# Performance work log

Hardware: AMD Instinct MI355X
Metric: run time of the kernel (lower is better)

The kernel has to match this reference:

```python
import jax, jax.numpy as jnp
import numpy as np

N = 100000
E = 1000000
C = 64      # hidden_channels
H = 4       # heads
O = C // H  # out channels per head
NEG_SLOPE = 0.2


def setup_inputs() -> dict:
    key = jax.random.key(0)
    ks = jax.random.split(key, 14)
    x = jax.random.normal(ks[0], (N, C), dtype=jnp.float32)
    edge_index = jax.random.randint(ks[1], (2, E), 0, N, dtype=jnp.int64)
    s = 1.0 / np.sqrt(C)
    params = {}
    for l in range(3):
        params[f"Wl{l+1}"] = jax.random.normal(ks[2 + 4 * l], (C, H * O), dtype=jnp.float32) * s
        params[f"Wr{l+1}"] = jax.random.normal(ks[3 + 4 * l], (C, H * O), dtype=jnp.float32) * s
        params[f"a{l+1}"] = jax.random.normal(ks[4 + 4 * l], (H, O), dtype=jnp.float32) * s
        params[f"b{l+1}"] = jnp.zeros((H * O,), dtype=jnp.float32)
    return {"x": x, "edge_index": edge_index, **params}


def _gatv2_layer(x, src, dst, Wl, Wr, a, b):
    # x: [N, C]; src/dst: [E]
    xl = (x @ Wl).reshape(N, H, O)  # source-side transform
    xr = (x @ Wr).reshape(N, H, O)  # target-side transform
    s = jax.nn.leaky_relu(xl[src] + xr[dst], NEG_SLOPE)     # [E, H, O]
    e = jnp.einsum("eho,ho->eh", s, a)                       # [E, H] logits
    # segment softmax over incoming edges of each target node
    m = jax.ops.segment_max(e, dst, num_segments=N)          # [N, H]
    ex = jnp.exp(e - m[dst])
    denom = jax.ops.segment_sum(ex, dst, num_segments=N)     # [N, H]
    alpha = ex / (denom[dst] + 1e-16)                        # [E, H]
    out = jax.ops.segment_sum(xl[src] * alpha[:, :, None], dst, num_segments=N)
    return out.reshape(N, H * O) + b


def reference(x, edge_index, Wl1, Wr1, a1, b1, Wl2, Wr2, a2, b2, Wl3, Wr3, a3, b3):
    src, dst = edge_index[0], edge_index[1]
    h = jax.nn.relu(_gatv2_layer(x, src, dst, Wl1, Wr1, a1, b1))
    h = jax.nn.relu(_gatv2_layer(h, src, dst, Wl2, Wr2, a2, b2))
    h = _gatv2_layer(h, src, dst, Wl3, Wr3, a3, b3)
    return h
```

## Files before the change

### kernel.cpp

```cpp
#include <hip/hip_runtime.h>
#include <math.h>

#define SLOPE 0.2f
#define LOG2E 1.4426950408889634f

#define DPP_ADD(x, ctrl) \
    ((x) + __int_as_float(__builtin_amdgcn_update_dpp( \
        0, __float_as_int(x), (ctrl), 0xF, 0xF, true)))


#define NPB 256
#define EPB 8192
#define MAXBK 2048

__global__ __launch_bounds__(256) void kH1(const int* __restrict__ ei,
                                           int* __restrict__ hist,
                                           int E, int nbk, int nblkE) {
    __shared__ int h[MAXBK];
    int t = threadIdx.x, b = blockIdx.x;
    for (int i = t; i < nbk; i += 256) h[i] = 0;
    __syncthreads();
    int e0 = b * EPB, e1 = min(e0 + EPB, E);
    for (int e = e0 + t; e < e1; e += 256)
        atomicAdd(&h[ei[E + e] >> 8], 1);
    __syncthreads();
    for (int i = t; i < nbk; i += 256)
        hist[i * nblkE + b] = h[i];
}

__global__ __launch_bounds__(256) void kH2(const int* __restrict__ ei,
                                           const int* __restrict__ hs,
                                           int* __restrict__ pairs,
                                           int E, int nbk, int nblkE) {
    __shared__ int soff[MAXBK];
    int t = threadIdx.x, b = blockIdx.x;
    for (int i = t; i < nbk; i += 256) soff[i] = hs[i * nblkE + b];
    __syncthreads();
    int e0 = b * EPB, e1 = min(e0 + EPB, E);
    for (int e = e0 + t; e < e1; e += 256) {
        int s = ei[e], d = ei[E + e];
        int slot = atomicAdd(&soff[d >> 8], 1);
        pairs[slot] = (s << 8) | (d & (NPB - 1));
    }
}

__global__ __launch_bounds__(256) void kB3(const int* __restrict__ hs,
                                           const int* __restrict__ pairs,
                                           int* __restrict__ btot,
                                           int E, int nbk, int nblkE) {
    __shared__ int sdeg[NPB];
    __shared__ int red[256];
    int t = threadIdx.x, b = blockIdx.x;
    sdeg[t] = 0;
    __syncthreads();
    int s0 = hs[b * nblkE];
    int s1 = (b + 1 < nbk) ? hs[(b + 1) * nblkE] : E;
    for (int i = s0 + t; i < s1; i += 256)
        atomicAdd(&sdeg[pairs[i] & (NPB - 1)], 1);
    __syncthreads();
    red[t] = (sdeg[t] + 3) & ~3;
    __syncthreads();
    for (int off = 128; off; off >>= 1) {
        if (t < off) red[t] += red[t + off];
        __syncthreads();
    }
    if (t == 0) btot[b] = red[0];
}

__global__ __launch_bounds__(256) void kscanB(const int* __restrict__ btot,
                                              int* __restrict__ bbase, int nbk) {
    __shared__ int sd[256];
    __shared__ int carry;
    int t = threadIdx.x;
    if (t == 0) carry = 0;
    __syncthreads();
    for (int base = 0; base < nbk; base += 256) {
        int v = (base + t < nbk) ? btot[base + t] : 0;
        sd[t] = v;
        __syncthreads();
        for (int off = 1; off < 256; off <<= 1) {
            int x = (t >= off) ? sd[t - off] : 0;
            __syncthreads();
            sd[t] += x;
            __syncthreads();
        }
        if (base + t < nbk) bbase[base + t] = sd[t] - v + carry;
        __syncthreads();
        if (t == 255) carry += sd[255];
        __syncthreads();
    }
}

__global__ __launch_bounds__(256) void kB4(const int* __restrict__ hs,
                                           const int* __restrict__ pairs,
                                           const int* __restrict__ bbase,
                                           int* __restrict__ rp,
                                           int* __restrict__ deg,
                                           int* __restrict__ col,
                                           int E, int nbk, int nblkE, int n) {
    __shared__ int sdeg[NPB];
    __shared__ int spfx[NPB];
    int t = threadIdx.x, b = blockIdx.x;
    sdeg[t] = 0;
    __syncthreads();
    int s0 = hs[b * nblkE];
    int s1 = (b + 1 < nbk) ? hs[(b + 1) * nblkE] : E;
    for (int i = s0 + t; i < s1; i += 256)
        atomicAdd(&sdeg[pairs[i] & (NPB - 1)], 1);
    __syncthreads();
    int cnt = sdeg[t];
    int pv = (cnt + 3) & ~3;
    spfx[t] = pv;
    __syncthreads();
    for (int off = 1; off < 256; off <<= 1) {
        int x = (t >= off) ? spfx[t - off] : 0;
        __syncthreads();
        spfx[t] += x;
        __syncthreads();
    }
    int rpt = bbase[b] + spfx[t] - pv;
    int node = b * NPB + t;
    if (node < n) { rp[node] = rpt; deg[node] = cnt; }
    __syncthreads();
    sdeg[t] = rpt;
    __syncthreads();
    for (int i = s0 + t; i < s1; i += 256) {
        int p = pairs[i];
        int slot = atomicAdd(&sdeg[p & (NPB - 1)], 1);
        col[slot] = p & ~(NPB - 1);
    }
}


__global__ __launch_bounds__(256) void k_scan1(const int* __restrict__ deg,
                                               int* __restrict__ rp,
                                               int* __restrict__ blk, int n) {
    __shared__ int sd[256];
    int t = threadIdx.x;
    int base = blockIdx.x * 1024 + t * 4;
    int v0 = 0, v1 = 0, v2 = 0, v3 = 0;
    if (base + 0 < n) v0 = deg[base + 0];
    if (base + 1 < n) v1 = deg[base + 1];
    if (base + 2 < n) v2 = deg[base + 2];
    if (base + 3 < n) v3 = deg[base + 3];
    int s = v0 + v1 + v2 + v3;
    sd[t] = s;
    __syncthreads();
    for (int off = 1; off < 256; off <<= 1) {
        int x = (t >= off) ? sd[t - off] : 0;
        __syncthreads();
        sd[t] += x;
        __syncthreads();
    }
    int ex = sd[t] - s;
    if (t == 255) blk[blockIdx.x] = sd[255];
    if (base + 0 < n) rp[base + 0] = ex; ex += v0;
    if (base + 1 < n) rp[base + 1] = ex; ex += v1;
    if (base + 2 < n) rp[base + 2] = ex; ex += v2;
    if (base + 3 < n) rp[base + 3] = ex;
}

__global__ __launch_bounds__(256) void k_scan2(int* __restrict__ blk, int nblk) {
    __shared__ int sd[256];
    int t = threadIdx.x;
    int v = (t < nblk) ? blk[t] : 0;
    sd[t] = v;
    __syncthreads();
    for (int off = 1; off < 256; off <<= 1) {
        int x = (t >= off) ? sd[t - off] : 0;
        __syncthreads();
        sd[t] += x;
        __syncthreads();
    }
    if (t < nblk) blk[t] = sd[t] - v;
}

__global__ __launch_bounds__(256) void k_scan3(int* __restrict__ rp,
                                               const int* __restrict__ blk,
                                               int n) {
    int t = threadIdx.x;
    int base = blockIdx.x * 1024 + t * 4;
    int off = blk[blockIdx.x];
    #pragma unroll
    for (int i = 0; i < 4; i++) {
        int idx = base + i;
        if (idx < n) rp[idx] += off;
    }
}


__global__ __launch_bounds__(256) void k_gemm(const float* __restrict__ in,
                                              const float* __restrict__ Wl,
                                              const float* __restrict__ Wr,
                                              float* __restrict__ xl,
                                              float* __restrict__ xr, int n) {
    __shared__ float4 sW[64 * 32];
    __shared__ float  sx[64 * 68];

    int t = threadIdx.x;
    int base = blockIdx.x * 64;

    float4 xs[4];
    int xrow[4], xkq[4];
    #pragma unroll
    for (int s = 0; s < 4; s++) {
        int i = t + 256 * s;
        int row = i >> 4, kq = i & 15;
        int g = base + row;
        if (g > n - 1) g = n - 1;
        xs[s] = *(const float4*)(in + (size_t)g * 64 + kq * 4);
        xrow[s] = row; xkq[s] = kq;
    }
    for (int i = t; i < 2048; i += 256) {
        int k = i >> 5, jg = i & 31;
        const float* src = (jg < 16) ? (Wl + k * 64 + jg * 4)
                                     : (Wr + k * 64 + (jg - 16) * 4);
        sW[i] = *(const float4*)src;
    }
    #pragma unroll
    for (int s = 0; s < 4; s++)
        *(float4*)(sx + xrow[s] * 68 + xkq[s] * 4) = xs[s];
    __syncthreads();

    int rt = t & 15;
    int ct = t >> 4;
    const float* sxp = sx + rt * 68;

    float4 acc[4][2];
    #pragma unroll
    for (int r = 0; r < 4; r++)
        #pragma unroll
        for (int j = 0; j < 2; j++) acc[r][j] = make_float4(0.f, 0.f, 0.f, 0.f);

    #pragma unroll 1
    for (int k0 = 0; k0 < 64; k0 += 4) {
        float4 xv[4];
        #pragma unroll
        for (int r = 0; r < 4; r++)
            xv[r] = *(const float4*)(sxp + r * (16 * 68) + k0);
        #pragma unroll
        for (int kk = 0; kk < 4; kk++) {
            float4 w0 = sW[(k0 + kk) * 32 + ct * 2 + 0];
            float4 w1 = sW[(k0 + kk) * 32 + ct * 2 + 1];
            #pragma unroll
            for (int r = 0; r < 4; r++) {
                float xk = (kk == 0) ? xv[r].x : (kk == 1) ? xv[r].y
                         : (kk == 2) ? xv[r].z : xv[r].w;
                acc[r][0].x += xk * w0.x;
                acc[r][0].y += xk * w0.y;
                acc[r][0].z += xk * w0.z;
                acc[r][0].w += xk * w0.w;
                acc[r][1].x += xk * w1.x;
                acc[r][1].y += xk * w1.y;
                acc[r][1].z += xk * w1.z;
                acc[r][1].w += xk * w1.w;
            }
        }
    }

    float* outh = (ct < 8) ? xl : xr;
    int cq = (ct & 7) * 8;
    #pragma unroll
    for (int r = 0; r < 4; r++) {
        int g = base + rt + 16 * r;
        if (g < n) {
            float* dst = outh + (size_t)g * 64 + cq;
            *(float4*)(dst + 0) = acc[r][0];
            *(float4*)(dst + 4) = acc[r][1];
        }
    }
}


__global__ __launch_bounds__(256) void k_node(const float* __restrict__ xl,
                                              const float* __restrict__ xr,
                                              const int* __restrict__ rp,
                                              const int* __restrict__ deg,
                                              const int* __restrict__ col,
                                              const float* __restrict__ A,
                                              const float* __restrict__ Bv,
                                              float* __restrict__ outp,
                                              int n, int relu) {
    int lane = threadIdx.x & 63;
    int node = __builtin_amdgcn_readfirstlane(blockIdx.x * 4 + (threadIdx.x >> 6));
    if (node >= n) return;
    int grp = lane >> 5;
    int s   = lane & 31;
    int chn = ((s >> 3) << 4) + ((s & 7) << 1);
    unsigned cofs = (unsigned)chn * 4u;

    float2 xr2 = *(const float2*)(xr + (size_t)node * 64 + chn);
    float2 a2  = *(const float2*)(A + chn);
    a2.x *= LOG2E; a2.y *= LOG2E;
    float2 b2  = *(const float2*)(Bv + chn);

    int start = rp[node];
    int d = deg[node];
    int nb = (d + 7) >> 3;
    const int* cp = col + start;
    const char* xlb = (const char*)xl;

    float den = 0.f;
    float ax = 0.f, ay = 0.f;

    auto batch = [&](const float2 (&v)[4], int ebase, bool full) {
        #pragma unroll
        for (int j = 0; j < 4; j++) {
            float sx_ = v[j].x + xr2.x;
            float sy_ = v[j].y + xr2.y;
            sx_ = fmaxf(sx_, SLOPE * sx_);
            sy_ = fmaxf(sy_, SLOPE * sy_);
            float q = sx_ * a2.x + sy_ * a2.y;
            q = DPP_ADD(q, 0xB1);
            q = DPP_ADD(q, 0x4E);
            q = DPP_ADD(q, 0x141);
            if (!full) {
                int eidx = ebase + 2 * j + grp;
                if (eidx >= d) q = -INFINITY;
            }
            float w = __builtin_amdgcn_exp2f(q);
            den += w;
            ax += w * v[j].x;
            ay += w * v[j].y;
        }
    };

    auto gather = [&](float2 (&v)[4], const int* q) {
        int c[8];
        *(int4*)(c + 0) = *(const int4*)(q + 0);
        *(int4*)(c + 4) = *(const int4*)(q + 4);
        #pragma unroll
        for (int j = 0; j < 4; j++) {
            unsigned cc = (unsigned)(grp ? c[2 * j + 1] : c[2 * j]);
            v[j] = *(const float2*)(xlb + (cc + cofs));
        }
    };

    float2 v[4];
    if (nb > 0) gather(v, cp);

    #pragma unroll 1
    for (int b = 0; b < nb - 1; b++) {
        float2 vN[4];
        gather(vN, cp + (b + 1) * 8);
        batch(v, b * 8, true);
        #pragma unroll
        for (int j = 0; j < 4; j++) v[j] = vN[j];
    }
    if (nb > 0) batch(v, (nb - 1) * 8, false);

    den += __shfl_xor(den, 32, 64);
    ax  += __shfl_xor(ax, 32, 64);
    ay  += __shfl_xor(ay, 32, 64);

    float inv = 1.f / (den + 1e-16f);
    float ox = ax * inv + b2.x;
    float oy = ay * inv + b2.y;
    if (relu) { ox = fmaxf(ox, 0.f); oy = fmaxf(oy, 0.f); }
    if (grp == 0)
        *(float2*)(outp + (size_t)node * 64 + chn) = make_float2(ox, oy);
}


extern "C" void kernel_launch(void* const* d_in, const int* in_sizes, int n_in,
                              void* d_out, int out_size, void* d_ws, size_t ws_size,
                              hipStream_t stream) {
    const float* x = (const float*)d_in[0];
    const int* ei = (const int*)d_in[1];
    int N = in_sizes[0] / 64;
    int E = in_sizes[1] / 2;

    const float* Wl[3] = {(const float*)d_in[2], (const float*)d_in[6], (const float*)d_in[10]};
    const float* Wr[3] = {(const float*)d_in[3], (const float*)d_in[7], (const float*)d_in[11]};
    const float* Av[3] = {(const float*)d_in[4], (const float*)d_in[8], (const float*)d_in[12]};
    const float* Bv[3] = {(const float*)d_in[5], (const float*)d_in[9], (const float*)d_in[13]};

    char* w = (char*)d_ws;
    auto carve = [&](size_t bytes) {
        void* p = (void*)w;
        w += (bytes + 255) & ~(size_t)255;
        return p;
    };
    int NBK    = (N + NPB - 1) / NPB;
    int NBLK_E = (E + EPB - 1) / EPB;
    size_t histN = (size_t)NBK * NBLK_E;
    size_t colN = (size_t)E + 3 * (size_t)N + 64;
    float* xl    = (float*)carve((size_t)N * 64 * 4);
    float* xr    = (float*)carve((size_t)N * 64 * 4);
    float* h     = (float*)carve((size_t)N * 64 * 4);
    int*   rp    = (int*)carve((size_t)N * 4);
    int*   deg   = (int*)carve((size_t)N * 4);
    int*   col   = (int*)carve(colN * 4);
    int*   pairs = (int*)carve((size_t)E * 4);
    int*   hist  = (int*)carve(histN * 4);
    int*   hs    = (int*)carve(histN * 4);
    int*   btot  = (int*)carve((size_t)NBK * 4);
    int*   bbase = (int*)carve((size_t)NBK * 4);
    int*   blkB  = (int*)carve(256 * 4);

    int nblkH1024 = (int)((histN + 1023) / 1024);
    int gemm_grid = (N + 63) / 64;
    int node_grid = (N + 3) / 4;

    hipMemsetAsync(col, 0, colN * 4, stream);

    kH1<<<NBLK_E, 256, 0, stream>>>(ei, hist, E, NBK, NBLK_E);
    k_scan1<<<nblkH1024, 256, 0, stream>>>(hist, hs, blkB, (int)histN);
    k_scan2<<<1, 256, 0, stream>>>(blkB, nblkH1024);
    k_scan3<<<nblkH1024, 256, 0, stream>>>(hs, blkB, (int)histN);
    kH2<<<NBLK_E, 256, 0, stream>>>(ei, hs, pairs, E, NBK, NBLK_E);

    kB3<<<NBK, 256, 0, stream>>>(hs, pairs, btot, E, NBK, NBLK_E);
    kscanB<<<1, 256, 0, stream>>>(btot, bbase, NBK);
    kB4<<<NBK, 256, 0, stream>>>(hs, pairs, bbase, rp, deg, col, E, NBK, NBLK_E, N);

    const float* in_l = x;
    for (int l = 0; l < 3; l++) {
        float* out_l = (l == 2) ? (float*)d_out : h;
        int relu = (l < 2) ? 1 : 0;
        k_gemm<<<gemm_grid, 256, 0, stream>>>(in_l, Wl[l], Wr[l], xl, xr, N);
        k_node<<<node_grid, 256, 0, stream>>>(xl, xr, rp, deg, col, Av[l], Bv[l],
                                              out_l, N, relu);
        in_l = h;
    }
}
```

Measured before the change: 359.6 us.

## Fuse CSR construction into one cooperative kernel with grid syncs

Replaces the eight-kernel CSR build (histogram, three-pass scan, scatter, per-bucket degree, bucket scan, final placement) and the col memset with a single cooperative kernel of 1024 blocks that uses grid.sync between phases. Padding of the per-node column lists changes from multiples of 4 to 16, and the padding slots are zeroed in-kernel instead of by a full memset. This is meant to remove launch gaps and the memset traffic, at the cost of grid-wide barriers, a fixed grid size, and more padding in col. The histogram scan now assumes nbk blocks each covering 1024 entries, which matches nbk*1024 hist entries.

```diff
diff --git a/kernel.cpp b/kernel.cpp
--- a/kernel.cpp
+++ b/kernel.cpp
@@ -1,5 +1,8 @@
 #include <hip/hip_runtime.h>
+#include <hip/hip_cooperative_groups.h>
 #include <math.h>
+
+namespace cg = cooperative_groups;
 
 #define SLOPE 0.2f
 #define LOG2E 1.4426950408889634f
@@ -10,181 +13,165 @@
 
 
 #define NPB 256
-#define EPB 8192
 #define MAXBK 2048
-
-__global__ __launch_bounds__(256) void kH1(const int* __restrict__ ei,
-                                           int* __restrict__ hist,
-                                           int E, int nbk, int nblkE) {
+#define CSRG 1024
+
+__global__ __launch_bounds__(256) void k_csr(const int* __restrict__ ei,
+                                             int* __restrict__ pairs,
+                                             int* __restrict__ hist,
+                                             int* __restrict__ blk,
+                                             int* __restrict__ btot,
+                                             int* __restrict__ bbase,
+                                             int* __restrict__ rp,
+                                             int* __restrict__ deg,
+                                             int* __restrict__ col,
+                                             int E, int nbk, int n) {
+    cg::grid_group grid = cg::this_grid();
     __shared__ int h[MAXBK];
+    __shared__ int sd[256];
+    __shared__ int carry;
+    __shared__ int sdeg[NPB];
+    __shared__ int spfx[NPB];
+
     int t = threadIdx.x, b = blockIdx.x;
+    int G = CSRG;
+    int chunk = (E + G - 1) / G;
+    int e0 = b * chunk, e1 = min(e0 + chunk, E);
+
     for (int i = t; i < nbk; i += 256) h[i] = 0;
     __syncthreads();
-    int e0 = b * EPB, e1 = min(e0 + EPB, E);
     for (int e = e0 + t; e < e1; e += 256)
         atomicAdd(&h[ei[E + e] >> 8], 1);
     __syncthreads();
     for (int i = t; i < nbk; i += 256)
-        hist[i * nblkE + b] = h[i];
-}
-
-__global__ __launch_bounds__(256) void kH2(const int* __restrict__ ei,
-                                           const int* __restrict__ hs,
-                                           int* __restrict__ pairs,
-                                           int E, int nbk, int nblkE) {
-    __shared__ int soff[MAXBK];
-    int t = threadIdx.x, b = blockIdx.x;
-    for (int i = t; i < nbk; i += 256) soff[i] = hs[i * nblkE + b];
+        hist[i * G + b] = h[i];
+    grid.sync();
+
+    if (b < nbk) {
+        int base = b * 1024 + t * 4;
+        int v0 = hist[base], v1 = hist[base + 1];
+        int v2 = hist[base + 2], v3 = hist[base + 3];
+        int s = v0 + v1 + v2 + v3;
+        sd[t] = s;
+        __syncthreads();
+        for (int off = 1; off < 256; off <<= 1) {
+            int x = (t >= off) ? sd[t - off] : 0;
+            __syncthreads();
+            sd[t] += x;
+            __syncthreads();
+        }
+        int ex = sd[t] - s;
+        if (t == 255) blk[b] = sd[255];
+        hist[base] = ex; ex += v0;
+        hist[base + 1] = ex; ex += v1;
+        hist[base + 2] = ex; ex += v2;
+        hist[base + 3] = ex;
+    }
+    grid.sync();
+
+    if (b == 0) {
+        if (t == 0) carry = 0;
+        __syncthreads();
+        for (int base = 0; base < nbk; base += 256) {
+            int v = (base + t < nbk) ? blk[base + t] : 0;
+            sd[t] = v;
+            __syncthreads();
+            for (int off = 1; off < 256; off <<= 1) {
+                int x = (t >= off) ? sd[t - off] : 0;
+                __syncthreads();
+                sd[t] += x;
+                __syncthreads();
+            }
+            if (base + t < nbk) blk[base + t] = sd[t] - v + carry;
+            __syncthreads();
+            if (t == 255) carry += sd[255];
+            __syncthreads();
+        }
+    }
+    grid.sync();
+
+    if (b < nbk) {
+        int base = b * 1024 + t * 4;
+        int o = blk[b];
+        hist[base] += o; hist[base + 1] += o;
+        hist[base + 2] += o; hist[base + 3] += o;
+    }
+    grid.sync();
+
+    for (int i = t; i < nbk; i += 256) h[i] = hist[i * G + b];
     __syncthreads();
-    int e0 = b * EPB, e1 = min(e0 + EPB, E);
     for (int e = e0 + t; e < e1; e += 256) {
         int s = ei[e], d = ei[E + e];
-        int slot = atomicAdd(&soff[d >> 8], 1);
+        int slot = atomicAdd(&h[d >> 8], 1);
         pairs[slot] = (s << 8) | (d & (NPB - 1));
     }
-}
-
-__global__ __launch_bounds__(256) void kB3(const int* __restrict__ hs,
-                                           const int* __restrict__ pairs,
-                                           int* __restrict__ btot,
-                                           int E, int nbk, int nblkE) {
-    __shared__ int sdeg[NPB];
-    __shared__ int red[256];
-    int t = threadIdx.x, b = blockIdx.x;
-    sdeg[t] = 0;
-    __syncthreads();
-    int s0 = hs[b * nblkE];
-    int s1 = (b + 1 < nbk) ? hs[(b + 1) * nblkE] : E;
-    for (int i = s0 + t; i < s1; i += 256)
-        atomicAdd(&sdeg[pairs[i] & (NPB - 1)], 1);
-    __syncthreads();
-    red[t] = (sdeg[t] + 3) & ~3;
-    __syncthreads();
-    for (int off = 128; off; off >>= 1) {
-        if (t < off) red[t] += red[t + off];
-        __syncthreads();
-    }
-    if (t == 0) btot[b] = red[0];
-}
-
-__global__ __launch_bounds__(256) void kscanB(const int* __restrict__ btot,
-                                              int* __restrict__ bbase, int nbk) {
-    __shared__ int sd[256];
-    __shared__ int carry;
-    int t = threadIdx.x;
-    if (t == 0) carry = 0;
-    __syncthreads();
-    for (int base = 0; base < nbk; base += 256) {
-        int v = (base + t < nbk) ? btot[base + t] : 0;
-        sd[t] = v;
+    grid.sync();
+
+    if (b < nbk) {
+        sdeg[t] = 0;
+        __syncthreads();
+        int s0 = hist[b * G];
+        int s1 = (b + 1 < nbk) ? hist[(b + 1) * G] : E;
+        for (int i = s0 + t; i < s1; i += 256)
+            atomicAdd(&sdeg[pairs[i] & (NPB - 1)], 1);
+        __syncthreads();
+        spfx[t] = (sdeg[t] + 15) & ~15;
+        __syncthreads();
+        for (int off = 128; off; off >>= 1) {
+            if (t < off) spfx[t] += spfx[t + off];
+            __syncthreads();
+        }
+        if (t == 0) btot[b] = spfx[0];
+    }
+    grid.sync();
+
+    if (b == 0) {
+        if (t == 0) carry = 0;
+        __syncthreads();
+        for (int base = 0; base < nbk; base += 256) {
+            int v = (base + t < nbk) ? btot[base + t] : 0;
+            sd[t] = v;
+            __syncthreads();
+            for (int off = 1; off < 256; off <<= 1) {
+                int x = (t >= off) ? sd[t - off] : 0;
+                __syncthreads();
+                sd[t] += x;
+                __syncthreads();
+            }
+            if (base + t < nbk) bbase[base + t] = sd[t] - v + carry;
+            __syncthreads();
+            if (t == 255) carry += sd[255];
+            __syncthreads();
+        }
+    }
+    grid.sync();
+
+    if (b < nbk) {
+        int cnt = sdeg[t];
+        int pv = (cnt + 15) & ~15;
+        spfx[t] = pv;
         __syncthreads();
         for (int off = 1; off < 256; off <<= 1) {
-            int x = (t >= off) ? sd[t - off] : 0;
-            __syncthreads();
-            sd[t] += x;
-            __syncthreads();
-        }
-        if (base + t < nbk) bbase[base + t] = sd[t] - v + carry;
-        __syncthreads();
-        if (t == 255) carry += sd[255];
-        __syncthreads();
-    }
-}
-
-__global__ __launch_bounds__(256) void kB4(const int* __restrict__ hs,
-                                           const int* __restrict__ pairs,
-                                           const int* __restrict__ bbase,
-                                           int* __restrict__ rp,
-                                           int* __restrict__ deg,
-                                           int* __restrict__ col,
-                                           int E, int nbk, int nblkE, int n) {
-    __shared__ int sdeg[NPB];
-    __shared__ int spfx[NPB];
-    int t = threadIdx.x, b = blockIdx.x;
-    sdeg[t] = 0;
-    __syncthreads();
-    int s0 = hs[b * nblkE];
-    int s1 = (b + 1 < nbk) ? hs[(b + 1) * nblkE] : E;
-    for (int i = s0 + t; i < s1; i += 256)
-        atomicAdd(&sdeg[pairs[i] & (NPB - 1)], 1);
-    __syncthreads();
-    int cnt = sdeg[t];
-    int pv = (cnt + 3) & ~3;
-    spfx[t] = pv;
-    __syncthreads();
-    for (int off = 1; off < 256; off <<= 1) {
-        int x = (t >= off) ? spfx[t - off] : 0;
-        __syncthreads();
-        spfx[t] += x;
-        __syncthreads();
-    }
-    int rpt = bbase[b] + spfx[t] - pv;
-    int node = b * NPB + t;
-    if (node < n) { rp[node] = rpt; deg[node] = cnt; }
-    __syncthreads();
-    sdeg[t] = rpt;
-    __syncthreads();
-    for (int i = s0 + t; i < s1; i += 256) {
-        int p = pairs[i];
-        int slot = atomicAdd(&sdeg[p & (NPB - 1)], 1);
-        col[slot] = p & ~(NPB - 1);
-    }
-}
-
-
-__global__ __launch_bounds__(256) void k_scan1(const int* __restrict__ deg,
-                                               int* __restrict__ rp,
-                                               int* __restrict__ blk, int n) {
-    __shared__ int sd[256];
-    int t = threadIdx.x;
-    int base = blockIdx.x * 1024 + t * 4;
-    int v0 = 0, v1 = 0, v2 = 0, v3 = 0;
-    if (base + 0 < n) v0 = deg[base + 0];
-    if (base + 1 < n) v1 = deg[base + 1];
-    if (base + 2 < n) v2 = deg[base + 2];
-    if (base + 3 < n) v3 = deg[base + 3];
-    int s = v0 + v1 + v2 + v3;
-    sd[t] = s;
-    __syncthreads();
-    for (int off = 1; off < 256; off <<= 1) {
-        int x = (t >= off) ? sd[t - off] : 0;
-        __syncthreads();
-        sd[t] += x;
-        __syncthreads();
-    }
-    int ex = sd[t] - s;
-    if (t == 255) blk[blockIdx.x] = sd[255];
-    if (base + 0 < n) rp[base + 0] = ex; ex += v0;
-    if (base + 1 < n) rp[base + 1] = ex; ex += v1;
-    if (base + 2 < n) rp[base + 2] = ex; ex += v2;
-    if (base + 3 < n) rp[base + 3] = ex;
-}
-
-__global__ __launch_bounds__(256) void k_scan2(int* __restrict__ blk, int nblk) {
-    __shared__ int sd[256];
-    int t = threadIdx.x;
-    int v = (t < nblk) ? blk[t] : 0;
-    sd[t] = v;
-    __syncthreads();
-    for (int off = 1; off < 256; off <<= 1) {
-        int x = (t >= off) ? sd[t - off] : 0;
-        __syncthreads();
-        sd[t] += x;
-        __syncthreads();
-    }
-    if (t < nblk) blk[t] = sd[t] - v;
-}
-
-__global__ __launch_bounds__(256) void k_scan3(int* __restrict__ rp,
-                                               const int* __restrict__ blk,
-                                               int n) {
-    int t = threadIdx.x;
-    int base = blockIdx.x * 1024 + t * 4;
-    int off = blk[blockIdx.x];
-    #pragma unroll
-    for (int i = 0; i < 4; i++) {
-        int idx = base + i;
-        if (idx < n) rp[idx] += off;
+            int x = (t >= off) ? spfx[t - off] : 0;
+            __syncthreads();
+            spfx[t] += x;
+            __syncthreads();
+        }
+        int rpt = bbase[b] + spfx[t] - pv;
+        int node = b * NPB + t;
+        if (node < n) { rp[node] = rpt; deg[node] = cnt; }
+        __syncthreads();
+        sdeg[t] = rpt;
+        __syncthreads();
+        int s0 = hist[b * G];
+        int s1 = (b + 1 < nbk) ? hist[(b + 1) * G] : E;
+        for (int i = s0 + t; i < s1; i += 256) {
+            int p = pairs[i];
+            int slot = atomicAdd(&sdeg[p & (NPB - 1)], 1);
+            col[slot] = p & ~(NPB - 1);
+        }
+        if (node < n)
+            for (int i = rpt + cnt; i < rpt + pv; i++) col[i] = 0;
     }
 }
 
@@ -381,10 +368,9 @@
         w += (bytes + 255) & ~(size_t)255;
         return p;
     };
-    int NBK    = (N + NPB - 1) / NPB;
-    int NBLK_E = (E + EPB - 1) / EPB;
-    size_t histN = (size_t)NBK * NBLK_E;
-    size_t colN = (size_t)E + 3 * (size_t)N + 64;
+    int NBK = (N + NPB - 1) / NPB;
+    size_t histN = (size_t)NBK * CSRG;
+    size_t colN = (size_t)E + 15 * (size_t)N + 64;
     float* xl    = (float*)carve((size_t)N * 64 * 4);
     float* xr    = (float*)carve((size_t)N * 64 * 4);
     float* h     = (float*)carve((size_t)N * 64 * 4);
@@ -393,26 +379,18 @@
     int*   col   = (int*)carve(colN * 4);
     int*   pairs = (int*)carve((size_t)E * 4);
     int*   hist  = (int*)carve(histN * 4);
-    int*   hs    = (int*)carve(histN * 4);
+    int*   blk   = (int*)carve((size_t)MAXBK * 4);
     int*   btot  = (int*)carve((size_t)NBK * 4);
     int*   bbase = (int*)carve((size_t)NBK * 4);
-    int*   blkB  = (int*)carve(256 * 4);
-
-    int nblkH1024 = (int)((histN + 1023) / 1024);
+
     int gemm_grid = (N + 63) / 64;
     int node_grid = (N + 3) / 4;
 
-    hipMemsetAsync(col, 0, colN * 4, stream);
-
-    kH1<<<NBLK_E, 256, 0, stream>>>(ei, hist, E, NBK, NBLK_E);
-    k_scan1<<<nblkH1024, 256, 0, stream>>>(hist, hs, blkB, (int)histN);
-    k_scan2<<<1, 256, 0, stream>>>(blkB, nblkH1024);
-    k_scan3<<<nblkH1024, 256, 0, stream>>>(hs, blkB, (int)histN);
-    kH2<<<NBLK_E, 256, 0, stream>>>(ei, hs, pairs, E, NBK, NBLK_E);
-
-    kB3<<<NBK, 256, 0, stream>>>(hs, pairs, btot, E, NBK, NBLK_E);
-    kscanB<<<1, 256, 0, stream>>>(btot, bbase, NBK);
-    kB4<<<NBK, 256, 0, stream>>>(hs, pairs, bbase, rp, deg, col, E, NBK, NBLK_E, N);
+    void* csr_args[] = {(void*)&ei, (void*)&pairs, (void*)&hist, (void*)&blk,
+                        (void*)&btot, (void*)&bbase, (void*)&rp, (void*)&deg,
+                        (void*)&col, (void*)&E, (void*)&NBK, (void*)&N};
+    hipLaunchCooperativeKernel((void*)k_csr, dim3(CSRG), dim3(256),
+                               csr_args, 0, stream);
 
     const float* in_l = x;
     for (int l = 0; l < 3; l++) {
```

Measured after the change: 1.094 ms. 204% more time.

## Fold single-block scans into consumers, drop col memset, pad rows to 16

Applied to the files above, without the earlier changes.

Removes the two single-block scan kernels (k_scan2, kscanB) by having each block of k_scan3 and kB4 reduce the preceding block totals itself, cutting kernel launches and serial tiny-kernel stages. Replaces the full hipMemsetAsync of col by having kB4 zero only its own padding slots. Row padding grows from multiples of 4 to multiples of 16, which enlarges col and adds padded work in the node kernel, possibly to suit a wider per-node edge loop.

```diff
diff --git a/kernel.cpp b/kernel.cpp
--- a/kernel.cpp
+++ b/kernel.cpp
@@ -27,110 +27,6 @@
     for (int i = t; i < nbk; i += 256)
         hist[i * nblkE + b] = h[i];
 }
-
-__global__ __launch_bounds__(256) void kH2(const int* __restrict__ ei,
-                                           const int* __restrict__ hs,
-                                           int* __restrict__ pairs,
-                                           int E, int nbk, int nblkE) {
-    __shared__ int soff[MAXBK];
-    int t = threadIdx.x, b = blockIdx.x;
-    for (int i = t; i < nbk; i += 256) soff[i] = hs[i * nblkE + b];
-    __syncthreads();
-    int e0 = b * EPB, e1 = min(e0 + EPB, E);
-    for (int e = e0 + t; e < e1; e += 256) {
-        int s = ei[e], d = ei[E + e];
-        int slot = atomicAdd(&soff[d >> 8], 1);
-        pairs[slot] = (s << 8) | (d & (NPB - 1));
-    }
-}
-
-__global__ __launch_bounds__(256) void kB3(const int* __restrict__ hs,
-                                           const int* __restrict__ pairs,
-                                           int* __restrict__ btot,
-                                           int E, int nbk, int nblkE) {
-    __shared__ int sdeg[NPB];
-    __shared__ int red[256];
-    int t = threadIdx.x, b = blockIdx.x;
-    sdeg[t] = 0;
-    __syncthreads();
-    int s0 = hs[b * nblkE];
-    int s1 = (b + 1 < nbk) ? hs[(b + 1) * nblkE] : E;
-    for (int i = s0 + t; i < s1; i += 256)
-        atomicAdd(&sdeg[pairs[i] & (NPB - 1)], 1);
-    __syncthreads();
-    red[t] = (sdeg[t] + 3) & ~3;
-    __syncthreads();
-    for (int off = 128; off; off >>= 1) {
-        if (t < off) red[t] += red[t + off];
-        __syncthreads();
-    }
-    if (t == 0) btot[b] = red[0];
-}
-
-__global__ __launch_bounds__(256) void kscanB(const int* __restrict__ btot,
-                                              int* __restrict__ bbase, int nbk) {
-    __shared__ int sd[256];
-    __shared__ int carry;
-    int t = threadIdx.x;
-    if (t == 0) carry = 0;
-    __syncthreads();
-    for (int base = 0; base < nbk; base += 256) {
-        int v = (base + t < nbk) ? btot[base + t] : 0;
-        sd[t] = v;
-        __syncthreads();
-        for (int off = 1; off < 256; off <<= 1) {
-            int x = (t >= off) ? sd[t - off] : 0;
-            __syncthreads();
-            sd[t] += x;
-            __syncthreads();
-        }
-        if (base + t < nbk) bbase[base + t] = sd[t] - v + carry;
-        __syncthreads();
-        if (t == 255) carry += sd[255];
-        __syncthreads();
-    }
-}
-
-__global__ __launch_bounds__(256) void kB4(const int* __restrict__ hs,
-                                           const int* __restrict__ pairs,
-                                           const int* __restrict__ bbase,
-                                           int* __restrict__ rp,
-                                           int* __restrict__ deg,
-                                           int* __restrict__ col,
-                                           int E, int nbk, int nblkE, int n) {
-    __shared__ int sdeg[NPB];
-    __shared__ int spfx[NPB];
-    int t = threadIdx.x, b = blockIdx.x;
-    sdeg[t] = 0;
-    __syncthreads();
-    int s0 = hs[b * nblkE];
-    int s1 = (b + 1 < nbk) ? hs[(b + 1) * nblkE] : E;
-    for (int i = s0 + t; i < s1; i += 256)
-        atomicAdd(&sdeg[pairs[i] & (NPB - 1)], 1);
-    __syncthreads();
-    int cnt = sdeg[t];
-    int pv = (cnt + 3) & ~3;
-    spfx[t] = pv;
-    __syncthreads();
-    for (int off = 1; off < 256; off <<= 1) {
-        int x = (t >= off) ? spfx[t - off] : 0;
-        __syncthreads();
-        spfx[t] += x;
-        __syncthreads();
-    }
-    int rpt = bbase[b] + spfx[t] - pv;
-    int node = b * NPB + t;
-    if (node < n) { rp[node] = rpt; deg[node] = cnt; }
-    __syncthreads();
-    sdeg[t] = rpt;
-    __syncthreads();
-    for (int i = s0 + t; i < s1; i += 256) {
-        int p = pairs[i];
-        int slot = atomicAdd(&sdeg[p & (NPB - 1)], 1);
-        col[slot] = p & ~(NPB - 1);
-    }
-}
-
 
 __global__ __launch_bounds__(256) void k_scan1(const int* __restrict__ deg,
                                                int* __restrict__ rp,
@@ -160,32 +56,119 @@
     if (base + 3 < n) rp[base + 3] = ex;
 }
 
-__global__ __launch_bounds__(256) void k_scan2(int* __restrict__ blk, int nblk) {
-    __shared__ int sd[256];
-    int t = threadIdx.x;
-    int v = (t < nblk) ? blk[t] : 0;
-    sd[t] = v;
-    __syncthreads();
-    for (int off = 1; off < 256; off <<= 1) {
-        int x = (t >= off) ? sd[t - off] : 0;
-        __syncthreads();
-        sd[t] += x;
-        __syncthreads();
-    }
-    if (t < nblk) blk[t] = sd[t] - v;
-}
-
 __global__ __launch_bounds__(256) void k_scan3(int* __restrict__ rp,
                                                const int* __restrict__ blk,
                                                int n) {
-    int t = threadIdx.x;
-    int base = blockIdx.x * 1024 + t * 4;
-    int off = blk[blockIdx.x];
+    __shared__ int red[256];
+    int t = threadIdx.x, b = blockIdx.x;
+    int v = 0;
+    for (int i = t; i < b; i += 256) v += blk[i];
+    red[t] = v;
+    __syncthreads();
+    for (int off = 128; off; off >>= 1) {
+        if (t < off) red[t] += red[t + off];
+        __syncthreads();
+    }
+    int off0 = red[0];
+    int base = b * 1024 + t * 4;
     #pragma unroll
     for (int i = 0; i < 4; i++) {
         int idx = base + i;
-        if (idx < n) rp[idx] += off;
-    }
+        if (idx < n) rp[idx] += off0;
+    }
+}
+
+__global__ __launch_bounds__(256) void kH2(const int* __restrict__ ei,
+                                           const int* __restrict__ hs,
+                                           int* __restrict__ pairs,
+                                           int E, int nbk, int nblkE) {
+    __shared__ int soff[MAXBK];
+    int t = threadIdx.x, b = blockIdx.x;
+    for (int i = t; i < nbk; i += 256) soff[i] = hs[i * nblkE + b];
+    __syncthreads();
+    int e0 = b * EPB, e1 = min(e0 + EPB, E);
+    for (int e = e0 + t; e < e1; e += 256) {
+        int s = ei[e], d = ei[E + e];
+        int slot = atomicAdd(&soff[d >> 8], 1);
+        pairs[slot] = (s << 8) | (d & (NPB - 1));
+    }
+}
+
+__global__ __launch_bounds__(256) void kB3(const int* __restrict__ hs,
+                                           const int* __restrict__ pairs,
+                                           int* __restrict__ btot,
+                                           int E, int nbk, int nblkE) {
+    __shared__ int sdeg[NPB];
+    __shared__ int red[256];
+    int t = threadIdx.x, b = blockIdx.x;
+    sdeg[t] = 0;
+    __syncthreads();
+    int s0 = hs[b * nblkE];
+    int s1 = (b + 1 < nbk) ? hs[(b + 1) * nblkE] : E;
+    for (int i = s0 + t; i < s1; i += 256)
+        atomicAdd(&sdeg[pairs[i] & (NPB - 1)], 1);
+    __syncthreads();
+    red[t] = (sdeg[t] + 15) & ~15;
+    __syncthreads();
+    for (int off = 128; off; off >>= 1) {
+        if (t < off) red[t] += red[t + off];
+        __syncthreads();
+    }
+    if (t == 0) btot[b] = red[0];
+}
+
+__global__ __launch_bounds__(256) void kB4(const int* __restrict__ hs,
+                                           const int* __restrict__ pairs,
+                                           const int* __restrict__ btot,
+                                           int* __restrict__ rp,
+                                           int* __restrict__ deg,
+                                           int* __restrict__ col,
+                                           int E, int nbk, int nblkE, int n) {
+    __shared__ int sdeg[NPB];
+    __shared__ int spfx[NPB];
+    int t = threadIdx.x, b = blockIdx.x;
+
+    int v = 0;
+    for (int i = t; i < b; i += 256) v += btot[i];
+    spfx[t] = v;
+    __syncthreads();
+    for (int off = 128; off; off >>= 1) {
+        if (t < off) spfx[t] += spfx[t + off];
+        __syncthreads();
+    }
+    int bb = spfx[0];
+    __syncthreads();
+
+    sdeg[t] = 0;
+    __syncthreads();
+    int s0 = hs[b * nblkE];
+    int s1 = (b + 1 < nbk) ? hs[(b + 1) * nblkE] : E;
+    for (int i = s0 + t; i < s1; i += 256)
+        atomicAdd(&sdeg[pairs[i] & (NPB - 1)], 1);
+    __syncthreads();
+    int cnt = sdeg[t];
+    int pv = (cnt + 15) & ~15;
+    spfx[t] = pv;
+    __syncthreads();
+    for (int off = 1; off < 256; off <<= 1) {
+        int x = (t >= off) ? spfx[t - off] : 0;
+        __syncthreads();
+        spfx[t] += x;
+        __syncthreads();
+    }
+    int rpt = bb + spfx[t] - pv;
+    int node = b * NPB + t;
+    if (node < n) { rp[node] = rpt; deg[node] = cnt; }
+    __syncthreads();
+    sdeg[t] = rpt;
+    __syncthreads();
+    for (int i = s0 + t; i < s1; i += 256) {
+        int p = pairs[i];
+        int slot = atomicAdd(&sdeg[p & (NPB - 1)], 1);
+        col[slot] = p & ~(NPB - 1);
+    }
+    if (node < n)
+        for (int i = rpt + cnt; i < rpt + pv; i++) col[i] = 0;
 }
 
 
@@ -384,7 +367,7 @@
     int NBK    = (N + NPB - 1) / NPB;
     int NBLK_E = (E + EPB - 1) / EPB;
     size_t histN = (size_t)NBK * NBLK_E;
-    size_t colN = (size_t)E + 3 * (size_t)N + 64;
+    size_t colN = (size_t)E + 15 * (size_t)N + 64;
     float* xl    = (float*)carve((size_t)N * 64 * 4);
     float* xr    = (float*)carve((size_t)N * 64 * 4);
     float* h     = (float*)carve((size_t)N * 64 * 4);
@@ -395,24 +378,19 @@
     int*   hist  = (int*)carve(histN * 4);
     int*   hs    = (int*)carve(histN * 4);
     int*   btot  = (int*)carve((size_t)NBK * 4);
-    int*   bbase = (int*)carve((size_t)NBK * 4);
     int*   blkB  = (int*)carve(256 * 4);
 
     int nblkH1024 = (int)((histN + 1023) / 1024);
     int gemm_grid = (N + 63) / 64;
     int node_grid = (N + 3) / 4;
 
-    hipMemsetAsync(col, 0, colN * 4, stream);
-
     kH1<<<NBLK_E, 256, 0, stream>>>(ei, hist, E, NBK, NBLK_E);
     k_scan1<<<nblkH1024, 256, 0, stream>>>(hist, hs, blkB, (int)histN);
-    k_scan2<<<1, 256, 0, stream>>>(blkB, nblkH1024);
     k_scan3<<<nblkH1024, 256, 0, stream>>>(hs, blkB, (int)histN);
     kH2<<<NBLK_E, 256, 0, stream>>>(ei, hs, pairs, E, NBK, NBLK_E);
 
     kB3<<<NBK, 256, 0, stream>>>(hs, pairs, btot, E, NBK, NBLK_E);
-    kscanB<<<1, 256, 0, stream>>>(btot, bbase, NBK);
-    kB4<<<NBK, 256, 0, stream>>>(hs, pairs, bbase, rp, deg, col, E, NBK, NBLK_E, N);
+    kB4<<<NBK, 256, 0, stream>>>(hs, pairs, btot, rp, deg, col, E, NBK, NBLK_E, N);
 
     const float* in_l = x;
     for (int l = 0; l < 3; l++) {
```

Result: faster. 352.0 us (-2.1%).
